# Kernel optimization log

Hardware: AMD Instinct MI355X
Metric: run time of the kernel (lower is better)

The kernel has to match this reference:

```python
import jax, jax.numpy as jnp
import numpy as np

FEATURES, HIDDEN, ITERS = 64, 128, 3
BS, N = 64, 512
TEMP = 0.01  # NegativeSquare temperature


def position_encoding_init(n_position, d):
    pos = np.arange(n_position)[:, None].astype(np.float64)
    j = np.arange(d)[None, :]
    enc = pos / np.power(10000.0, 2 * (j // 2) / d)
    enc[0] = 0.0
    enc[1:, 0::2] = np.sin(enc[1:, 0::2])
    enc[1:, 1::2] = np.cos(enc[1:, 1::2])
    return jnp.asarray(enc, jnp.float32)


def setup_inputs() -> dict:
    key = jax.random.key(0)
    ks = jax.random.split(key, 32)
    g = lambda k, shp: 0.02 * jax.random.normal(k, shp, dtype=jnp.float32)
    inp = {
        'x': jax.random.normal(ks[0], (BS, N, FEATURES), dtype=jnp.float32),
        'mask': jnp.ones((BS, N, N), dtype=jnp.float32),
        # content embedding (1-layer MLP features->hidden, relu)
        'W_emb': g(ks[1], (FEATURES, HIDDEN)), 'b_emb': jnp.zeros((HIDDEN,), jnp.float32),
        # sinusoid positional table (trainable Parameter in torch)
        'pos_table': position_encoding_init(1000, HIDDEN),
        # per-iteration MP layers (untied): message MLP + GRU vertex update
        'Wm': g(ks[2], (ITERS, HIDDEN, HIDDEN)), 'bm': jnp.zeros((ITERS, HIDDEN), jnp.float32),
        'Wz': g(ks[3], (ITERS, HIDDEN, HIDDEN)), 'Uz': g(ks[4], (ITERS, HIDDEN, HIDDEN)), 'bz': jnp.zeros((ITERS, HIDDEN), jnp.float32),
        'Wr': g(ks[5], (ITERS, HIDDEN, HIDDEN)), 'Ur': g(ks[6], (ITERS, HIDDEN, HIDDEN)), 'br': jnp.zeros((ITERS, HIDDEN), jnp.float32),
        'Wh': g(ks[7], (ITERS, HIDDEN, HIDDEN)), 'Uh': g(ks[8], (ITERS, HIDDEN, HIDDEN)), 'bh': jnp.zeros((ITERS, HIDDEN), jnp.float32),
        # positional GRUUpdate(hidden, 3): input h (hidden) -> state s (3)
        'Wpz': g(ks[9], (HIDDEN, 3)), 'Upz': g(ks[10], (3, 3)), 'bpz': jnp.zeros((3,), jnp.float32),
        'Wpr': g(ks[11], (HIDDEN, 3)), 'Upr': g(ks[12], (3, 3)), 'bpr': jnp.zeros((3,), jnp.float32),
        'Wph': g(ks[13], (HIDDEN, 3)), 'Uph': g(ks[14], (3, 3)), 'bph': jnp.zeros((3,), jnp.float32),
    }
    return inp


def _adj(s, mask):
    # NegativeSquare: exp(-||s_i - s_j||^2 / temperature) * mask
    sq = jnp.sum(s * s, axis=-1)  # [b, n]
    d2 = sq[:, :, None] + sq[:, None, :] - 2.0 * jnp.einsum('bid,bjd->bij', s, s)
    return jnp.exp(-d2 / TEMP) * mask


def _spatial_variable(bs, n):
    idx = (jnp.arange(n, dtype=jnp.float32) - (n - 1) / 2.0) / n
    s = jnp.stack([idx, jnp.zeros(n, jnp.float32), jnp.zeros(n, jnp.float32)], axis=-1)
    return jnp.broadcast_to(s[None], (bs, n, 3))


def reference(x, mask, W_emb, b_emb, pos_table, Wm, bm, Wz, Uz, bz, Wr, Ur, br,
              Wh, Uh, bh, Wpz, Upz, bpz, Wpr, Upr, bpr, Wph, Uph, bph):
    bs, n, _ = x.shape
    iters = Wm.shape[0]
    h = jax.nn.relu(jnp.einsum('bnf,fh->bnh', x, W_emb) + b_emb)
    h = h + pos_table[:n][None]  # pos = arange(n)
    s = _spatial_variable(bs, n)
    A = _adj(s, mask)
    for i in range(iters):
        # message passing layer i
        m = jax.nn.relu(jnp.einsum('bnh,hk->bnk', h, Wm[i]) + bm[i])
        agg = jnp.einsum('bij,bjh->bih', A, m)
        z = jax.nn.sigmoid(agg @ Wz[i] + h @ Uz[i] + bz[i])
        r = jax.nn.sigmoid(agg @ Wr[i] + h @ Ur[i] + br[i])
        hh = jnp.tanh(agg @ Wh[i] + (r * h) @ Uh[i] + bh[i])
        h = (1.0 - z) * h + z * hh
        # positional GRU update: input h, state s
        zs = jax.nn.sigmoid(h @ Wpz + s @ Upz + bpz)
        rs = jax.nn.sigmoid(h @ Wpr + s @ Upr + bpr)
        ss = jnp.tanh(h @ Wph + (rs * s) @ Uph + bph)
        s = (1.0 - zs) * s + zs * ss
        A = _adj(s, mask)
    return A
```

## Files before the change

kernel.cpp:

```cpp
#include <hip/hip_runtime.h>
#include <math.h>

#define BSZ  64
#define NSEQ 512
#define FEAT 64
#define HID  128
#define NITER 3
#define RTOT (BSZ*NSEQ)
#define LDAP 136

typedef __attribute__((ext_vector_type(8))) short bf16x8;
typedef __attribute__((ext_vector_type(4))) float f32x4;
typedef unsigned int u32;


__device__ __forceinline__ float sigm(float v) {
  v = fminf(fmaxf(v, -30.f), 30.f);
  return 1.0f / (1.0f + __expf(-v));
}
__device__ __forceinline__ float tanh_fast(float v) {
  v = fminf(fmaxf(v, -15.f), 15.f);
  float e = __expf(2.0f * v);
  return (e - 1.0f) / (e + 1.0f);
}

__device__ __forceinline__ u32 pack_split(float a) {
  u32 ub = __float_as_uint(a);
  u32 hi = ub >> 16;
  float res = a - __uint_as_float(hi << 16);
  u32 lo = __float_as_uint(res) >> 16;
  return (hi << 16) | lo;
}
__device__ __forceinline__ float bf2f(short v) {
  return __uint_as_float(((u32)(unsigned short)v) << 16);
}

__device__ __forceinline__ f32x4 mfma3(bf16x8 ah, bf16x8 al, bf16x8 bh, bf16x8 bl, f32x4 c) {
  c = __builtin_amdgcn_mfma_f32_16x16x32_bf16(ah, bh, c, 0, 0, 0);
  c = __builtin_amdgcn_mfma_f32_16x16x32_bf16(ah, bl, c, 0, 0, 0);
  c = __builtin_amdgcn_mfma_f32_16x16x32_bf16(al, bh, c, 0, 0, 0);
  return c;
}

__device__ __forceinline__ void stage_planes(const u32* __restrict__ g, short* hiP, short* loP, int t) {
  const int row = t >> 3, col = (t & 7) * 16;
  const u32* src = g + (size_t)row * HID + col;
  #pragma unroll
  for (int i = 0; i < 4; ++i) {
    uint4 u = *(const uint4*)(src + i * 4);
    *(short4*)&hiP[row * LDAP + col + i * 4] =
        make_short4((short)(u.x >> 16), (short)(u.y >> 16), (short)(u.z >> 16), (short)(u.w >> 16));
    *(short4*)&loP[row * LDAP + col + i * 4] =
        make_short4((short)(u.x & 0xffff), (short)(u.y & 0xffff), (short)(u.z & 0xffff), (short)(u.w & 0xffff));
  }
}

#define GATE(ACC, AP, WB) do { \
  _Pragma("unroll") \
  for (int ks_ = 0; ks_ < 4; ++ks_) { \
    bf16x8 ah_ = *(bf16x8*)&P[AP][lrow][ks_*32 + kgrp]; \
    bf16x8 al_ = *(bf16x8*)&P[(AP)+1][lrow][ks_*32 + kgrp]; \
    _Pragma("unroll") \
    for (int nt_ = 0; nt_ < 4; ++nt_) { \
      const short* fb_ = (WB) + (((ks_*2 + nh)*4 + nt_) * 1024) + l * 8; \
      bf16x8 bh_ = *(const bf16x8*)fb_; \
      bf16x8 bl_ = *(const bf16x8*)(fb_ + 512); \
      ACC[nt_] = mfma3(ah_, al_, bh_, bl_, ACC[nt_]); \
    } \
  } \
} while (0)

__device__ __forceinline__ void micro4(const float4 a, const float4 b0, const float4 b1,
                                       const float4 b2, const float4 b3, float acc[4]) {
  acc[0] = fmaf(a.x, b0.x, acc[0]); acc[0] = fmaf(a.y, b1.x, acc[0]);
  acc[0] = fmaf(a.z, b2.x, acc[0]); acc[0] = fmaf(a.w, b3.x, acc[0]);
  acc[1] = fmaf(a.x, b0.y, acc[1]); acc[1] = fmaf(a.y, b1.y, acc[1]);
  acc[1] = fmaf(a.z, b2.y, acc[1]); acc[1] = fmaf(a.w, b3.y, acc[1]);
  acc[2] = fmaf(a.x, b0.z, acc[2]); acc[2] = fmaf(a.y, b1.z, acc[2]);
  acc[2] = fmaf(a.z, b2.z, acc[2]); acc[2] = fmaf(a.w, b3.z, acc[2]);
  acc[3] = fmaf(a.x, b0.w, acc[3]); acc[3] = fmaf(a.y, b1.w, acc[3]);
  acc[3] = fmaf(a.z, b2.w, acc[3]); acc[3] = fmaf(a.w, b3.w, acc[3]);
}


__global__ __launch_bounds__(256) void k_prep(
    const float* __restrict__ Wm, const float* __restrict__ Wz, const float* __restrict__ Uz,
    const float* __restrict__ Wr, const float* __restrict__ Ur, const float* __restrict__ Wh,
    const float* __restrict__ Uh, short* __restrict__ wpl) {
  __shared__ float Wl[HID * HID];
  const int t = threadIdx.x;
  const int m = blockIdx.x;
  const int g = m / 3, it = m - g * 3;
  const float* src;
  switch (g) { case 0: src = Wm; break; case 1: src = Wz; break; case 2: src = Uz; break;
               case 3: src = Wr; break; case 4: src = Ur; break; case 5: src = Wh; break;
               default: src = Uh; }
  src += (size_t)it * HID * HID;
  for (int i = t; i < HID * HID / 4; i += 256) ((float4*)Wl)[i] = ((const float4*)src)[i];
  __syncthreads();
  short* dst = wpl + (size_t)m * 32768;
  for (int s = t; s < 2048; s += 256) {
    const int lane = s & 63;
    const int blk = s >> 6;
    const int nt = blk & 3;
    const int nh = (blk >> 2) & 1;
    const int ks = blk >> 3;
    const int n = nh * 64 + nt * 16 + (lane & 15);
    const int k0 = ks * 32 + (lane >> 4) * 8;
    short h8[8], l8[8];
    #pragma unroll
    for (int j = 0; j < 8; ++j) {
      u32 pk = pack_split(Wl[(size_t)(k0 + j) * HID + n]);
      h8[j] = (short)(pk >> 16);
      l8[j] = (short)(pk & 0xffff);
    }
    short* o = dst + blk * 1024 + lane * 8;
    *(bf16x8*)o = *(bf16x8*)h8;
    *(bf16x8*)(o + 512) = *(bf16x8*)l8;
  }
}

__global__ __launch_bounds__(256) void k_embed(const float* __restrict__ x, const float* __restrict__ W,
                                               const float* __restrict__ bias, const float* __restrict__ pos,
                                               u32* __restrict__ hP) {
  __shared__ float xs[32][FEAT];
  const int t = threadIdx.x;
  const int row0 = blockIdx.x * 32;
  {
    const float4* xv = (const float4*)(x + (size_t)row0 * FEAT);
    float4* xd = (float4*)&xs[0][0];
    for (int i = t; i < 32 * FEAT / 4; i += 256) xd[i] = xv[i];
  }
  __syncthreads();
  const int c0 = (t & 31) * 4;
  const int r0 = (t >> 5) * 4;
  float acc[4][4] = {};
  #pragma unroll 2
  for (int k = 0; k < FEAT; k += 4) {
    float4 b0 = *(const float4*)&W[(k + 0) * HID + c0];
    float4 b1 = *(const float4*)&W[(k + 1) * HID + c0];
    float4 b2 = *(const float4*)&W[(k + 2) * HID + c0];
    float4 b3 = *(const float4*)&W[(k + 3) * HID + c0];
    float4 a0 = *(const float4*)&xs[r0 + 0][k];
    float4 a1 = *(const float4*)&xs[r0 + 1][k];
    float4 a2 = *(const float4*)&xs[r0 + 2][k];
    float4 a3 = *(const float4*)&xs[r0 + 3][k];
    micro4(a0, b0, b1, b2, b3, acc[0]);
    micro4(a1, b0, b1, b2, b3, acc[1]);
    micro4(a2, b0, b1, b2, b3, acc[2]);
    micro4(a3, b0, b1, b2, b3, acc[3]);
  }
  const float4 bv = *(const float4*)&bias[c0];
  #pragma unroll
  for (int r = 0; r < 4; ++r) {
    const int row = row0 + r0 + r;
    const int n = row & (NSEQ - 1);
    const float4 pv = *(const float4*)&pos[(size_t)n * HID + c0];
    uint4 pk;
    pk.x = pack_split(fmaxf(acc[r][0] + bv.x, 0.f) + pv.x);
    pk.y = pack_split(fmaxf(acc[r][1] + bv.y, 0.f) + pv.y);
    pk.z = pack_split(fmaxf(acc[r][2] + bv.z, 0.f) + pv.z);
    pk.w = pack_split(fmaxf(acc[r][3] + bv.w, 0.f) + pv.w);
    *(uint4*)&hP[(size_t)row * HID + c0] = pk;
  }
}

__global__ __launch_bounds__(256) void k_sinit(float* __restrict__ s) {
  const int i = blockIdx.x * 256 + threadIdx.x;
  if (i < RTOT) {
    const int n = i & (NSEQ - 1);
    s[(size_t)i * 3 + 0] = ((float)n - (NSEQ - 1) * 0.5f) / (float)NSEQ;
    s[(size_t)i * 3 + 1] = 0.f;
    s[(size_t)i * 3 + 2] = 0.f;
  }
}

__global__ __launch_bounds__(512) void k_msg(const u32* __restrict__ hP, const short* __restrict__ wpl,
                                             int iter, const float* __restrict__ bm,
                                             short* __restrict__ mtB) {
  __shared__ short P[2][64][LDAP];
  __shared__ short T[2][128][72];
  const int t = threadIdx.x;
  const int row0 = blockIdx.x * 64;
  stage_planes(hP + (size_t)row0 * HID, &P[0][0][0], &P[1][0][0], t);
  __syncthreads();
  const int l = t & 63, w = t >> 6;
  const int mt = w & 3, nh = w >> 2;
  const int lrow = mt * 16 + (l & 15);
  const int kgrp = (l >> 4) * 8;
  const int ncol = l & 15;
  f32x4 z4 = {0.f, 0.f, 0.f, 0.f};
  f32x4 acc[4];
  #pragma unroll
  for (int i = 0; i < 4; ++i) acc[i] = z4;
  GATE(acc, 0, wpl + (size_t)(0 * 3 + iter) * 32768);
  const int rbase = mt * 16 + (l >> 4) * 4;
  #pragma unroll
  for (int nt = 0; nt < 4; ++nt) {
    const int cc = nh * 64 + nt * 16 + ncol;
    const float bmc = bm[cc];
    #pragma unroll
    for (int q = 0; q < 4; ++q) {
      u32 pk = pack_split(fmaxf(acc[nt][q] + bmc, 0.f));
      T[0][cc][rbase + q] = (short)(pk >> 16);
      T[1][cc][rbase + q] = (short)(pk & 0xffff);
    }
  }
  __syncthreads();
  const int b = row0 >> 9, j0 = row0 & (NSEQ - 1);
  const int n = t >> 2, jq = (t & 3) * 16;
  const int nh2 = n >> 6, nt2 = (n >> 4) & 3;
  #pragma unroll
  for (int gch = 0; gch < 2; ++gch) {
    const int jj = jq + gch * 8;
    const int jt = (j0 + jj) >> 5;
    const int jjj = (j0 + jj) & 31;
    const int lane = (jjj >> 3) * 16 + (n & 15);
    #pragma unroll
    for (int pl = 0; pl < 2; ++pl) {
      size_t off = ((((((size_t)b * 16 + jt) * 2 + nh2) * 4 + nt2) * 2 + pl) * 64 + lane) * 8;
      *(bf16x8*)&mtB[off] = *(bf16x8*)&T[pl][n][jj];
    }
  }
}

__global__ __launch_bounds__(256) void k_agg(const float* __restrict__ s, const float* __restrict__ mask,
                                             const short* __restrict__ mtB, u32* __restrict__ aggP) {
  __shared__ float sj[NSEQ][3];
  __shared__ short WH2[2][32][40];
  __shared__ short WL2[2][32][40];
  const int t = threadIdx.x;
  const int b = blockIdx.x;
  const int i0 = blockIdx.y * 32;
  {
    const float* sp = s + (size_t)b * NSEQ * 3;
    for (int i = t; i < NSEQ * 3; i += 256) (&sj[0][0])[i] = sp[i];
  }
  __syncthreads();
  const float* maskb = mask + (size_t)b * NSEQ * NSEQ;
  const int wi = t >> 3, wj4 = (t & 7) * 4;
  const float six = sj[i0 + wi][0], siy = sj[i0 + wi][1], siz = sj[i0 + wi][2];
  {
    float4 mk = *(const float4*)&maskb[(size_t)(i0 + wi) * NSEQ + wj4];
    float vals[4] = {mk.x, mk.y, mk.z, mk.w};
    short ha[4], la[4];
    #pragma unroll
    for (int c = 0; c < 4; ++c) {
      const int jj = wj4 + c;
      float dx = six - sj[jj][0], dy = siy - sj[jj][1], dz = siz - sj[jj][2];
      u32 pk = pack_split(__expf(-100.0f * (dx * dx + dy * dy + dz * dz)) * vals[c]);
      ha[c] = (short)(pk >> 16); la[c] = (short)(pk & 0xffff);
    }
    *(short4*)&WH2[0][wi][wj4] = make_short4(ha[0], ha[1], ha[2], ha[3]);
    *(short4*)&WL2[0][wi][wj4] = make_short4(la[0], la[1], la[2], la[3]);
  }
  __syncthreads();
  const int l = t & 63, w = t >> 6;
  const int mt = w & 1, nh = w >> 1;
  const int kgrp = (l >> 4) * 8, ncol = l & 15;
  const int arow = mt * 16 + (l & 15);
  f32x4 z4 = {0.f, 0.f, 0.f, 0.f};
  f32x4 acc[4];
  #pragma unroll
  for (int i = 0; i < 4; ++i) acc[i] = z4;
  const short* mtb = mtB + (size_t)b * 131072;
  #pragma unroll 1
  for (int jt = 0; jt < 16; ++jt) {
    const int buf = jt & 1;
    const int jn = (jt + 1) * 32;
    float4 mkn;
    if (jt < 15) mkn = *(const float4*)&maskb[(size_t)(i0 + wi) * NSEQ + jn + wj4];
    bf16x8 ah = *(bf16x8*)&WH2[buf][arow][kgrp];
    bf16x8 al = *(bf16x8*)&WL2[buf][arow][kgrp];
    #pragma unroll
    for (int nt = 0; nt < 4; ++nt) {
      const short* fb = mtb + ((((size_t)jt * 2 + nh) * 4 + nt) * 2) * 512 + l * 8;
      acc[nt] = mfma3(ah, al, *(const bf16x8*)fb, *(const bf16x8*)(fb + 512), acc[nt]);
    }
    if (jt < 15) {
      float vals[4] = {mkn.x, mkn.y, mkn.z, mkn.w};
      short ha[4], la[4];
      #pragma unroll
      for (int c = 0; c < 4; ++c) {
        const int jj = jn + wj4 + c;
        float dx = six - sj[jj][0], dy = siy - sj[jj][1], dz = siz - sj[jj][2];
        u32 pk = pack_split(__expf(-100.0f * (dx * dx + dy * dy + dz * dz)) * vals[c]);
        ha[c] = (short)(pk >> 16); la[c] = (short)(pk & 0xffff);
      }
      *(short4*)&WH2[buf ^ 1][wi][wj4] = make_short4(ha[0], ha[1], ha[2], ha[3]);
      *(short4*)&WL2[buf ^ 1][wi][wj4] = make_short4(la[0], la[1], la[2], la[3]);
    }
    __syncthreads();
  }
  #pragma unroll
  for (int nt = 0; nt < 4; ++nt) {
    const int cc = nh * 64 + nt * 16 + ncol;
    #pragma unroll
    for (int q = 0; q < 4; ++q) {
      const int grow = i0 + mt * 16 + (l >> 4) * 4 + q;
      aggP[((size_t)b * NSEQ + grow) * HID + cc] = pack_split(acc[nt][q]);
    }
  }
}

__global__ __launch_bounds__(512) void k_zrc(
    const u32* __restrict__ aggP, u32* __restrict__ hP,
    const short* __restrict__ wpl, int iter,
    const float* __restrict__ bz, const float* __restrict__ br, const float* __restrict__ bhh) {
  __shared__ short P[4][64][LDAP];
  const int t = threadIdx.x;
  const int row0 = blockIdx.x * 64;
  stage_planes(aggP + (size_t)row0 * HID, &P[0][0][0], &P[1][0][0], t);
  stage_planes(hP + (size_t)row0 * HID, &P[2][0][0], &P[3][0][0], t);
  __syncthreads();
  const int l = t & 63, w = t >> 6;
  const int mt = w & 3, nh = w >> 2;
  const int lrow = mt * 16 + (l & 15);
  const int kgrp = (l >> 4) * 8;
  const int ncol = l & 15;
  f32x4 z4 = {0.f, 0.f, 0.f, 0.f};
  f32x4 accz[4], accr[4];
  #pragma unroll
  for (int i = 0; i < 4; ++i) { accz[i] = z4; accr[i] = z4; }
  #pragma unroll 1
  for (int g = 0; g < 4; ++g) {
    const short* WB = wpl + (size_t)((g + 1) * 3 + iter) * 32768;
    const int ap = (g & 1) * 2;
    if (g < 2) { GATE(accz, ap, WB); }
    else       { GATE(accr, ap, WB); }
  }
  const int rbase = mt * 16 + (l >> 4) * 4;
  float hreg[4][4];
  float rhv[4][4];
  #pragma unroll
  for (int nt = 0; nt < 4; ++nt) {
    const int cc = nh * 64 + nt * 16 + ncol;
    const float brc = br[cc];
    #pragma unroll
    for (int q = 0; q < 4; ++q) {
      float hv = bf2f(P[2][rbase + q][cc]) + bf2f(P[3][rbase + q][cc]);
      hreg[nt][q] = hv;
      rhv[nt][q] = sigm(accr[nt][q] + brc) * hv;
    }
  }
  __syncthreads();
  #pragma unroll
  for (int nt = 0; nt < 4; ++nt) {
    const int cc = nh * 64 + nt * 16 + ncol;
    #pragma unroll
    for (int q = 0; q < 4; ++q) {
      u32 pk = pack_split(rhv[nt][q]);
      P[2][rbase + q][cc] = (short)(pk >> 16);
      P[3][rbase + q][cc] = (short)(pk & 0xffff);
    }
  }
  __syncthreads();
  #pragma unroll
  for (int i = 0; i < 4; ++i) accr[i] = z4;
  GATE(accr, 0, wpl + (size_t)(5 * 3 + iter) * 32768);
  GATE(accr, 2, wpl + (size_t)(6 * 3 + iter) * 32768);
  #pragma unroll
  for (int nt = 0; nt < 4; ++nt) {
    const int cc = nh * 64 + nt * 16 + ncol;
    const float bzc = bz[cc], bhc = bhh[cc];
    #pragma unroll
    for (int q = 0; q < 4; ++q) {
      float z = sigm(accz[nt][q] + bzc);
      float cand = tanh_fast(accr[nt][q] + bhc);
      float hn = (1.f - z) * hreg[nt][q] + z * cand;
      hP[(size_t)(row0 + rbase + q) * HID + cc] = pack_split(hn);
    }
  }
}

__global__ __launch_bounds__(256) void k_posgru(const u32* __restrict__ hP, float* __restrict__ s,
    const float* __restrict__ Wpz, const float* __restrict__ Upz, const float* __restrict__ bpz,
    const float* __restrict__ Wpr, const float* __restrict__ Upr, const float* __restrict__ bpr,
    const float* __restrict__ Wph, const float* __restrict__ Uph, const float* __restrict__ bph) {
  const int lane = threadIdx.x & 63;
  const int w = threadIdx.x >> 6;
  const int row = blockIdx.x * 4 + w;
  const int k0 = lane * 2;
  const uint2 hv2 = *(const uint2*)&hP[(size_t)row * HID + k0];
  const float hx = bf2f((short)(hv2.x >> 16)) + bf2f((short)(hv2.x & 0xffff));
  const float hy = bf2f((short)(hv2.y >> 16)) + bf2f((short)(hv2.y & 0xffff));
  float p[9];
  #pragma unroll
  for (int c = 0; c < 3; ++c) {
    p[c]     = hx * Wpz[k0 * 3 + c] + hy * Wpz[(k0 + 1) * 3 + c];
    p[3 + c] = hx * Wpr[k0 * 3 + c] + hy * Wpr[(k0 + 1) * 3 + c];
    p[6 + c] = hx * Wph[k0 * 3 + c] + hy * Wph[(k0 + 1) * 3 + c];
  }
  #pragma unroll
  for (int off = 32; off > 0; off >>= 1) {
    #pragma unroll
    for (int q = 0; q < 9; ++q) p[q] += __shfl_xor(p[q], off, 64);
  }
  const float s0 = s[(size_t)row * 3 + 0], s1 = s[(size_t)row * 3 + 1], s2 = s[(size_t)row * 3 + 2];
  float zs[3], rs[3], ss[3];
  #pragma unroll
  for (int c = 0; c < 3; ++c) {
    zs[c] = sigm(p[c]     + s0 * Upz[c] + s1 * Upz[3 + c] + s2 * Upz[6 + c] + bpz[c]);
    rs[c] = sigm(p[3 + c] + s0 * Upr[c] + s1 * Upr[3 + c] + s2 * Upr[6 + c] + bpr[c]);
  }
  const float t0 = rs[0] * s0, t1 = rs[1] * s1, t2 = rs[2] * s2;
  #pragma unroll
  for (int c = 0; c < 3; ++c)
    ss[c] = tanh_fast(p[6 + c] + t0 * Uph[c] + t1 * Uph[3 + c] + t2 * Uph[6 + c] + bph[c]);
  if (lane == 0) {
    s[(size_t)row * 3 + 0] = (1.f - zs[0]) * s0 + zs[0] * ss[0];
    s[(size_t)row * 3 + 1] = (1.f - zs[1]) * s1 + zs[1] * ss[1];
    s[(size_t)row * 3 + 2] = (1.f - zs[2]) * s2 + zs[2] * ss[2];
  }
}

__global__ __launch_bounds__(256) void k_finalA(const float* __restrict__ s, const float* __restrict__ mask,
                                                float* __restrict__ A) {
  __shared__ float sj[NSEQ][3];
  const int t = threadIdx.x;
  const int b = blockIdx.x;
  const int i0 = blockIdx.y * 16;
  {
    const float* sp = s + (size_t)b * NSEQ * 3;
    for (int i = t; i < NSEQ * 3; i += 256) (&sj[0][0])[i] = sp[i];
  }
  __syncthreads();
  #pragma unroll
  for (int p = 0; p < 8; ++p) {
    const int e = t + p * 256;
    const int ii = e >> 7;
    const int j4 = (e & 127) * 4;
    const float six = sj[i0 + ii][0], siy = sj[i0 + ii][1], siz = sj[i0 + ii][2];
    const size_t base = ((size_t)b * NSEQ + i0 + ii) * NSEQ + j4;
    const float4 mk = *(const float4*)&mask[base];
    float4 o;
    { float dx = six - sj[j4+0][0], dy = siy - sj[j4+0][1], dz = siz - sj[j4+0][2];
      o.x = __expf(-100.0f*(dx*dx + dy*dy + dz*dz)) * mk.x; }
    { float dx = six - sj[j4+1][0], dy = siy - sj[j4+1][1], dz = siz - sj[j4+1][2];
      o.y = __expf(-100.0f*(dx*dx + dy*dy + dz*dz)) * mk.y; }
    { float dx = six - sj[j4+2][0], dy = siy - sj[j4+2][1], dz = siz - sj[j4+2][2];
      o.z = __expf(-100.0f*(dx*dx + dy*dy + dz*dz)) * mk.z; }
    { float dx = six - sj[j4+3][0], dy = siy - sj[j4+3][1], dz = siz - sj[j4+3][2];
      o.w = __expf(-100.0f*(dx*dx + dy*dy + dz*dz)) * mk.w; }
    *(float4*)&A[base] = o;
  }
}


extern "C" void kernel_launch(void* const* d_in, const int* in_sizes, int n_in,
                              void* d_out, int out_size, void* d_ws, size_t ws_size,
                              hipStream_t stream) {
  const float* x      = (const float*)d_in[0];
  const float* mask   = (const float*)d_in[1];
  const float* W_emb  = (const float*)d_in[2];
  const float* b_emb  = (const float*)d_in[3];
  const float* pos    = (const float*)d_in[4];
  const float* Wm     = (const float*)d_in[5];
  const float* bm     = (const float*)d_in[6];
  const float* Wz     = (const float*)d_in[7];
  const float* Uz     = (const float*)d_in[8];
  const float* bz     = (const float*)d_in[9];
  const float* Wr     = (const float*)d_in[10];
  const float* Ur     = (const float*)d_in[11];
  const float* br     = (const float*)d_in[12];
  const float* Wh     = (const float*)d_in[13];
  const float* Uh     = (const float*)d_in[14];
  const float* bh     = (const float*)d_in[15];
  const float* Wpz    = (const float*)d_in[16];
  const float* Upz    = (const float*)d_in[17];
  const float* bpz    = (const float*)d_in[18];
  const float* Wpr    = (const float*)d_in[19];
  const float* Upr    = (const float*)d_in[20];
  const float* bpr    = (const float*)d_in[21];
  const float* Wph    = (const float*)d_in[22];
  const float* Uph    = (const float*)d_in[23];
  const float* bph    = (const float*)d_in[24];

  u32*   hP = (u32*)d_ws;
  float* s  = (float*)d_ws + (size_t)RTOT * HID;
  float* ob   = (float*)d_out;
  u32*   aggP = (u32*)ob;
  short* mtB  = (short*)(ob + (size_t)RTOT * HID);
  short* wpl  = mtB + (size_t)BSZ * 131072;

  k_prep<<<21, 256, 0, stream>>>(Wm, Wz, Uz, Wr, Ur, Wh, Uh, wpl);
  k_embed<<<RTOT / 32, 256, 0, stream>>>(x, W_emb, b_emb, pos, hP);
  k_sinit<<<RTOT / 256, 256, 0, stream>>>(s);

  for (int i = 0; i < NITER; ++i) {
    const size_t bo = (size_t)i * HID;
    k_msg<<<RTOT / 64, 512, 0, stream>>>(hP, wpl, i, bm + bo, mtB);
    k_agg<<<dim3(BSZ, NSEQ / 32), 256, 0, stream>>>(s, mask, mtB, aggP);
    k_zrc<<<RTOT / 64, 512, 0, stream>>>(aggP, hP, wpl, i, bz + bo, br + bo, bh + bo);
    k_posgru<<<RTOT / 4, 256, 0, stream>>>(hP, s, Wpz, Upz, bpz, Wpr, Upr, bpr, Wph, Uph, bph);
  }
  k_finalA<<<dim3(BSZ, NSEQ / 16), 256, 0, stream>>>(s, mask, (float*)d_out);
}
```

Before: 490.0 us.

## Compute adjacency A-fragments directly in registers, removing LDS staging and barriers

The aggregation kernel no longer builds adjacency tiles in shared memory with double buffering and a barrier per k-step. Each lane now computes the 8 adjacency values it needs for its MFMA A-operand straight into registers, reading the mask row directly, and the loop is unrolled by two. This removes the LDS writes and reads and the 16 __syncthreads. In exchange each exp is computed redundantly across the two waves that share an mt row-tile (4 waves, nh duplicates), roughly doubling the exp work, and the mask loads become per-lane strided float4 reads.

```diff
diff --git a/kernel.cpp b/kernel.cpp
--- a/kernel.cpp
+++ b/kernel.cpp
@@ -227,8 +227,6 @@
 __global__ __launch_bounds__(256) void k_agg(const float* __restrict__ s, const float* __restrict__ mask,
                                              const short* __restrict__ mtB, u32* __restrict__ aggP) {
   __shared__ float sj[NSEQ][3];
-  __shared__ short WH2[2][32][40];
-  __shared__ short WL2[2][32][40];
   const int t = threadIdx.x;
   const int b = blockIdx.x;
   const int i0 = blockIdx.y * 32;
@@ -237,60 +235,39 @@
     for (int i = t; i < NSEQ * 3; i += 256) (&sj[0][0])[i] = sp[i];
   }
   __syncthreads();
-  const float* maskb = mask + (size_t)b * NSEQ * NSEQ;
-  const int wi = t >> 3, wj4 = (t & 7) * 4;
-  const float six = sj[i0 + wi][0], siy = sj[i0 + wi][1], siz = sj[i0 + wi][2];
-  {
-    float4 mk = *(const float4*)&maskb[(size_t)(i0 + wi) * NSEQ + wj4];
-    float vals[4] = {mk.x, mk.y, mk.z, mk.w};
-    short ha[4], la[4];
-    #pragma unroll
-    for (int c = 0; c < 4; ++c) {
-      const int jj = wj4 + c;
-      float dx = six - sj[jj][0], dy = siy - sj[jj][1], dz = siz - sj[jj][2];
-      u32 pk = pack_split(__expf(-100.0f * (dx * dx + dy * dy + dz * dz)) * vals[c]);
-      ha[c] = (short)(pk >> 16); la[c] = (short)(pk & 0xffff);
-    }
-    *(short4*)&WH2[0][wi][wj4] = make_short4(ha[0], ha[1], ha[2], ha[3]);
-    *(short4*)&WL2[0][wi][wj4] = make_short4(la[0], la[1], la[2], la[3]);
-  }
-  __syncthreads();
   const int l = t & 63, w = t >> 6;
   const int mt = w & 1, nh = w >> 1;
   const int kgrp = (l >> 4) * 8, ncol = l & 15;
   const int arow = mt * 16 + (l & 15);
+  const float six = sj[i0 + arow][0], siy = sj[i0 + arow][1], siz = sj[i0 + arow][2];
+  const float* mrow = mask + ((size_t)b * NSEQ + i0 + arow) * NSEQ;
   f32x4 z4 = {0.f, 0.f, 0.f, 0.f};
   f32x4 acc[4];
   #pragma unroll
   for (int i = 0; i < 4; ++i) acc[i] = z4;
   const short* mtb = mtB + (size_t)b * 131072;
-  #pragma unroll 1
+  #pragma unroll 2
   for (int jt = 0; jt < 16; ++jt) {
-    const int buf = jt & 1;
-    const int jn = (jt + 1) * 32;
-    float4 mkn;
-    if (jt < 15) mkn = *(const float4*)&maskb[(size_t)(i0 + wi) * NSEQ + jn + wj4];
-    bf16x8 ah = *(bf16x8*)&WH2[buf][arow][kgrp];
-    bf16x8 al = *(bf16x8*)&WL2[buf][arow][kgrp];
+    const int j0 = jt * 32 + kgrp;
+    const float4 mk0 = *(const float4*)&mrow[j0];
+    const float4 mk1 = *(const float4*)&mrow[j0 + 4];
+    const float mv[8] = {mk0.x, mk0.y, mk0.z, mk0.w, mk1.x, mk1.y, mk1.z, mk1.w};
+    short ha[8], la[8];
+    #pragma unroll
+    for (int j = 0; j < 8; ++j) {
+      const int jj = j0 + j;
+      const float dx = six - sj[jj][0], dy = siy - sj[jj][1], dz = siz - sj[jj][2];
+      const u32 pk = pack_split(__expf(-100.0f * (dx * dx + dy * dy + dz * dz)) * mv[j]);
+      ha[j] = (short)(pk >> 16);
+      la[j] = (short)(pk & 0xffff);
+    }
+    const bf16x8 ah = *(bf16x8*)ha;
+    const bf16x8 al = *(bf16x8*)la;
     #pragma unroll
     for (int nt = 0; nt < 4; ++nt) {
       const short* fb = mtb + ((((size_t)jt * 2 + nh) * 4 + nt) * 2) * 512 + l * 8;
       acc[nt] = mfma3(ah, al, *(const bf16x8*)fb, *(const bf16x8*)(fb + 512), acc[nt]);
     }
-    if (jt < 15) {
-      float vals[4] = {mkn.x, mkn.y, mkn.z, mkn.w};
-      short ha[4], la[4];
-      #pragma unroll
-      for (int c = 0; c < 4; ++c) {
-        const int jj = jn + wj4 + c;
-        float dx = six - sj[jj][0], dy = siy - sj[jj][1], dz = siz - sj[jj][2];
-        u32 pk = pack_split(__expf(-100.0f * (dx * dx + dy * dy + dz * dz)) * vals[c]);
-        ha[c] = (short)(pk >> 16); la[c] = (short)(pk & 0xffff);
-      }
-      *(short4*)&WH2[buf ^ 1][wi][wj4] = make_short4(ha[0], ha[1], ha[2], ha[3]);
-      *(short4*)&WL2[buf ^ 1][wi][wj4] = make_short4(la[0], la[1], la[2], la[3]);
-    }
-    __syncthreads();
   }
   #pragma unroll
   for (int nt = 0; nt < 4; ++nt) {
```

Result: slower. 525.0 us (+7.1%).

## Fuse positional GRU into gate kernel and halve aggregation row tile

Applied to the files above, without the earlier changes.

The positional GRU update is folded into the end of k_zrc. The new h is restaged into shared memory and reduced there by 8-thread groups per row, which removes a separate kernel launch and a global re-read of h. Separately, k_agg now processes 16 rows per block instead of 32, doubling the grid. Each wave computes two output tiles instead of four. This adds parallelism but rereads the message operand twice as often and recomputes the adjacency tile with narrower stores.

```diff
diff --git a/kernel.cpp b/kernel.cpp
--- a/kernel.cpp
+++ b/kernel.cpp
@@ -227,78 +227,74 @@
 __global__ __launch_bounds__(256) void k_agg(const float* __restrict__ s, const float* __restrict__ mask,
                                              const short* __restrict__ mtB, u32* __restrict__ aggP) {
   __shared__ float sj[NSEQ][3];
-  __shared__ short WH2[2][32][40];
-  __shared__ short WL2[2][32][40];
+  __shared__ short WH2[2][16][40];
+  __shared__ short WL2[2][16][40];
   const int t = threadIdx.x;
   const int b = blockIdx.x;
-  const int i0 = blockIdx.y * 32;
+  const int i0 = blockIdx.y * 16;
   {
     const float* sp = s + (size_t)b * NSEQ * 3;
     for (int i = t; i < NSEQ * 3; i += 256) (&sj[0][0])[i] = sp[i];
   }
   __syncthreads();
   const float* maskb = mask + (size_t)b * NSEQ * NSEQ;
-  const int wi = t >> 3, wj4 = (t & 7) * 4;
+  const int wi = t >> 4, wj2 = (t & 15) * 2;
   const float six = sj[i0 + wi][0], siy = sj[i0 + wi][1], siz = sj[i0 + wi][2];
   {
-    float4 mk = *(const float4*)&maskb[(size_t)(i0 + wi) * NSEQ + wj4];
-    float vals[4] = {mk.x, mk.y, mk.z, mk.w};
-    short ha[4], la[4];
-    #pragma unroll
-    for (int c = 0; c < 4; ++c) {
-      const int jj = wj4 + c;
+    float2 mk = *(const float2*)&maskb[(size_t)(i0 + wi) * NSEQ + wj2];
+    float vals[2] = {mk.x, mk.y};
+    #pragma unroll
+    for (int c = 0; c < 2; ++c) {
+      const int jj = wj2 + c;
       float dx = six - sj[jj][0], dy = siy - sj[jj][1], dz = siz - sj[jj][2];
       u32 pk = pack_split(__expf(-100.0f * (dx * dx + dy * dy + dz * dz)) * vals[c]);
-      ha[c] = (short)(pk >> 16); la[c] = (short)(pk & 0xffff);
-    }
-    *(short4*)&WH2[0][wi][wj4] = make_short4(ha[0], ha[1], ha[2], ha[3]);
-    *(short4*)&WL2[0][wi][wj4] = make_short4(la[0], la[1], la[2], la[3]);
+      WH2[0][wi][jj] = (short)(pk >> 16);
+      WL2[0][wi][jj] = (short)(pk & 0xffff);
+    }
   }
   __syncthreads();
   const int l = t & 63, w = t >> 6;
-  const int mt = w & 1, nh = w >> 1;
+  const int nh = w & 1, ntp = w >> 1;
   const int kgrp = (l >> 4) * 8, ncol = l & 15;
-  const int arow = mt * 16 + (l & 15);
+  const int arow = l & 15;
   f32x4 z4 = {0.f, 0.f, 0.f, 0.f};
-  f32x4 acc[4];
-  #pragma unroll
-  for (int i = 0; i < 4; ++i) acc[i] = z4;
+  f32x4 acc[2];
+  acc[0] = z4; acc[1] = z4;
   const short* mtb = mtB + (size_t)b * 131072;
   #pragma unroll 1
   for (int jt = 0; jt < 16; ++jt) {
     const int buf = jt & 1;
     const int jn = (jt + 1) * 32;
-    float4 mkn;
-    if (jt < 15) mkn = *(const float4*)&maskb[(size_t)(i0 + wi) * NSEQ + jn + wj4];
+    float2 mkn;
+    if (jt < 15) mkn = *(const float2*)&maskb[(size_t)(i0 + wi) * NSEQ + jn + wj2];
     bf16x8 ah = *(bf16x8*)&WH2[buf][arow][kgrp];
     bf16x8 al = *(bf16x8*)&WL2[buf][arow][kgrp];
     #pragma unroll
-    for (int nt = 0; nt < 4; ++nt) {
+    for (int ntl = 0; ntl < 2; ++ntl) {
+      const int nt = ntp * 2 + ntl;
       const short* fb = mtb + ((((size_t)jt * 2 + nh) * 4 + nt) * 2) * 512 + l * 8;
-      acc[nt] = mfma3(ah, al, *(const bf16x8*)fb, *(const bf16x8*)(fb + 512), acc[nt]);
+      acc[ntl] = mfma3(ah, al, *(const bf16x8*)fb, *(const bf16x8*)(fb + 512), acc[ntl]);
     }
     if (jt < 15) {
-      float vals[4] = {mkn.x, mkn.y, mkn.z, mkn.w};
-      short ha[4], la[4];
+      float vals[2] = {mkn.x, mkn.y};
       #pragma unroll
-      for (int c = 0; c < 4; ++c) {
-        const int jj = jn + wj4 + c;
+      for (int c = 0; c < 2; ++c) {
+        const int jj = jn + wj2 + c;
         float dx = six - sj[jj][0], dy = siy - sj[jj][1], dz = siz - sj[jj][2];
         u32 pk = pack_split(__expf(-100.0f * (dx * dx + dy * dy + dz * dz)) * vals[c]);
-        ha[c] = (short)(pk >> 16); la[c] = (short)(pk & 0xffff);
+        WH2[buf ^ 1][wi][wj2 + c] = (short)(pk >> 16);
+        WL2[buf ^ 1][wi][wj2 + c] = (short)(pk & 0xffff);
       }
-      *(short4*)&WH2[buf ^ 1][wi][wj4] = make_short4(ha[0], ha[1], ha[2], ha[3]);
-      *(short4*)&WL2[buf ^ 1][wi][wj4] = make_short4(la[0], la[1], la[2], la[3]);
     }
     __syncthreads();
   }
   #pragma unroll
-  for (int nt = 0; nt < 4; ++nt) {
-    const int cc = nh * 64 + nt * 16 + ncol;
+  for (int ntl = 0; ntl < 2; ++ntl) {
+    const int cc = nh * 64 + (ntp * 2 + ntl) * 16 + ncol;
     #pragma unroll
     for (int q = 0; q < 4; ++q) {
-      const int grow = i0 + mt * 16 + (l >> 4) * 4 + q;
-      aggP[((size_t)b * NSEQ + grow) * HID + cc] = pack_split(acc[nt][q]);
+      const int grow = i0 + (l >> 4) * 4 + q;
+      aggP[((size_t)b * NSEQ + grow) * HID + cc] = pack_split(acc[ntl][q]);
     }
   }
 }
@@ -306,7 +302,11 @@
 __global__ __launch_bounds__(512) void k_zrc(
     const u32* __restrict__ aggP, u32* __restrict__ hP,
     const short* __restrict__ wpl, int iter,
-    const float* __restrict__ bz, const float* __restrict__ br, const float* __restrict__ bhh) {
+    const float* __restrict__ bz, const float* __restrict__ br, const float* __restrict__ bhh,
+    float* __restrict__ s,
+    const float* __restrict__ Wpz, const float* __restrict__ Upz, const float* __restrict__ bpz,
+    const float* __restrict__ Wpr, const float* __restrict__ Upr, const float* __restrict__ bpr,
+    const float* __restrict__ Wph, const float* __restrict__ Uph, const float* __restrict__ bph) {
   __shared__ short P[4][64][LDAP];
   const int t = threadIdx.x;
   const int row0 = blockIdx.x * 64;
@@ -359,6 +359,7 @@
   for (int i = 0; i < 4; ++i) accr[i] = z4;
   GATE(accr, 0, wpl + (size_t)(5 * 3 + iter) * 32768);
   GATE(accr, 2, wpl + (size_t)(6 * 3 + iter) * 32768);
+  float hn_[4][4];
   #pragma unroll
   for (int nt = 0; nt < 4; ++nt) {
     const int cc = nh * 64 + nt * 16 + ncol;
@@ -368,46 +369,53 @@
       float z = sigm(accz[nt][q] + bzc);
       float cand = tanh_fast(accr[nt][q] + bhc);
       float hn = (1.f - z) * hreg[nt][q] + z * cand;
+      hn_[nt][q] = hn;
       hP[(size_t)(row0 + rbase + q) * HID + cc] = pack_split(hn);
     }
   }
-}
-
-__global__ __launch_bounds__(256) void k_posgru(const u32* __restrict__ hP, float* __restrict__ s,
-    const float* __restrict__ Wpz, const float* __restrict__ Upz, const float* __restrict__ bpz,
-    const float* __restrict__ Wpr, const float* __restrict__ Upr, const float* __restrict__ bpr,
-    const float* __restrict__ Wph, const float* __restrict__ Uph, const float* __restrict__ bph) {
-  const int lane = threadIdx.x & 63;
-  const int w = threadIdx.x >> 6;
-  const int row = blockIdx.x * 4 + w;
-  const int k0 = lane * 2;
-  const uint2 hv2 = *(const uint2*)&hP[(size_t)row * HID + k0];
-  const float hx = bf2f((short)(hv2.x >> 16)) + bf2f((short)(hv2.x & 0xffff));
-  const float hy = bf2f((short)(hv2.y >> 16)) + bf2f((short)(hv2.y & 0xffff));
-  float p[9];
-  #pragma unroll
-  for (int c = 0; c < 3; ++c) {
-    p[c]     = hx * Wpz[k0 * 3 + c] + hy * Wpz[(k0 + 1) * 3 + c];
-    p[3 + c] = hx * Wpr[k0 * 3 + c] + hy * Wpr[(k0 + 1) * 3 + c];
-    p[6 + c] = hx * Wph[k0 * 3 + c] + hy * Wph[(k0 + 1) * 3 + c];
-  }
-  #pragma unroll
-  for (int off = 32; off > 0; off >>= 1) {
+  __syncthreads();
+  #pragma unroll
+  for (int nt = 0; nt < 4; ++nt) {
+    const int cc = nh * 64 + nt * 16 + ncol;
+    #pragma unroll
+    for (int q = 0; q < 4; ++q) {
+      u32 pk = pack_split(hn_[nt][q]);
+      P[0][rbase + q][cc] = (short)(pk >> 16);
+      P[1][rbase + q][cc] = (short)(pk & 0xffff);
+    }
+  }
+  __syncthreads();
+  const int prow = t >> 3, sub = t & 7;
+  float p[9] = {0.f, 0.f, 0.f, 0.f, 0.f, 0.f, 0.f, 0.f, 0.f};
+  #pragma unroll 4
+  for (int kk = 0; kk < 16; ++kk) {
+    const int k = sub * 16 + kk;
+    const float hv = bf2f(P[0][prow][k]) + bf2f(P[1][prow][k]);
+    #pragma unroll
+    for (int c = 0; c < 3; ++c) {
+      p[c]     = fmaf(hv, Wpz[k * 3 + c], p[c]);
+      p[3 + c] = fmaf(hv, Wpr[k * 3 + c], p[3 + c]);
+      p[6 + c] = fmaf(hv, Wph[k * 3 + c], p[6 + c]);
+    }
+  }
+  #pragma unroll
+  for (int off = 1; off <= 4; off <<= 1) {
     #pragma unroll
     for (int q = 0; q < 9; ++q) p[q] += __shfl_xor(p[q], off, 64);
   }
-  const float s0 = s[(size_t)row * 3 + 0], s1 = s[(size_t)row * 3 + 1], s2 = s[(size_t)row * 3 + 2];
-  float zs[3], rs[3], ss[3];
-  #pragma unroll
-  for (int c = 0; c < 3; ++c) {
-    zs[c] = sigm(p[c]     + s0 * Upz[c] + s1 * Upz[3 + c] + s2 * Upz[6 + c] + bpz[c]);
-    rs[c] = sigm(p[3 + c] + s0 * Upr[c] + s1 * Upr[3 + c] + s2 * Upr[6 + c] + bpr[c]);
-  }
-  const float t0 = rs[0] * s0, t1 = rs[1] * s1, t2 = rs[2] * s2;
-  #pragma unroll
-  for (int c = 0; c < 3; ++c)
-    ss[c] = tanh_fast(p[6 + c] + t0 * Uph[c] + t1 * Uph[3 + c] + t2 * Uph[6 + c] + bph[c]);
-  if (lane == 0) {
+  if (sub == 0) {
+    const int row = row0 + prow;
+    const float s0 = s[(size_t)row * 3 + 0], s1 = s[(size_t)row * 3 + 1], s2 = s[(size_t)row * 3 + 2];
+    float zs[3], rs[3], ss[3];
+    #pragma unroll
+    for (int c = 0; c < 3; ++c) {
+      zs[c] = sigm(p[c]     + s0 * Upz[c] + s1 * Upz[3 + c] + s2 * Upz[6 + c] + bpz[c]);
+      rs[c] = sigm(p[3 + c] + s0 * Upr[c] + s1 * Upr[3 + c] + s2 * Upr[6 + c] + bpr[c]);
+    }
+    const float t0 = rs[0] * s0, t1 = rs[1] * s1, t2 = rs[2] * s2;
+    #pragma unroll
+    for (int c = 0; c < 3; ++c)
+      ss[c] = tanh_fast(p[6 + c] + t0 * Uph[c] + t1 * Uph[3 + c] + t2 * Uph[6 + c] + bph[c]);
     s[(size_t)row * 3 + 0] = (1.f - zs[0]) * s0 + zs[0] * ss[0];
     s[(size_t)row * 3 + 1] = (1.f - zs[1]) * s1 + zs[1] * ss[1];
     s[(size_t)row * 3 + 2] = (1.f - zs[2]) * s2 + zs[2] * ss[2];
@@ -490,9 +498,9 @@
   for (int i = 0; i < NITER; ++i) {
     const size_t bo = (size_t)i * HID;
     k_msg<<<RTOT / 64, 512, 0, stream>>>(hP, wpl, i, bm + bo, mtB);
-    k_agg<<<dim3(BSZ, NSEQ / 32), 256, 0, stream>>>(s, mask, mtB, aggP);
-    k_zrc<<<RTOT / 64, 512, 0, stream>>>(aggP, hP, wpl, i, bz + bo, br + bo, bh + bo);
-    k_posgru<<<RTOT / 4, 256, 0, stream>>>(hP, s, Wpz, Upz, bpz, Wpr, Upr, bpr, Wph, Uph, bph);
+    k_agg<<<dim3(BSZ, NSEQ / 16), 256, 0, stream>>>(s, mask, mtB, aggP);
+    k_zrc<<<RTOT / 64, 512, 0, stream>>>(aggP, hP, wpl, i, bz + bo, br + bo, bh + bo,
+                                         s, Wpz, Upz, bpz, Wpr, Upr, bpr, Wph, Uph, bph);
   }
   k_finalA<<<dim3(BSZ, NSEQ / 16), 256, 0, stream>>>(s, mask, (float*)d_out);
 }
```

New measurement: 473.2 us. 1.04x faster.
